# Optimization experiments

Measured on AMD Instinct MI355X. Metric: run time of the kernel, lower is better.

The kernel has to match this reference:

```python
import math
import jax, jax.numpy as jnp
import numpy as np

B, L, DIM, H = 2, 2048, 1024, 16
D = DIM // H  # head_dim = 64
EPS = 1e-6


def setup_inputs() -> dict:
    key = jax.random.key(0)
    ks = jax.random.split(key, 5)
    s = 0.02
    return {
        "x": jax.random.normal(ks[0], (B, L, DIM), jnp.float32),
        "pe": jax.random.normal(ks[1], (B, 1, L, D // 2, 2, 2), jnp.float32),
        "w_qkv": jax.random.normal(ks[2], (DIM, 3 * DIM), jnp.float32) * s,
        "q_scale": jnp.ones((D,), jnp.float32),
        "k_scale": jnp.ones((D,), jnp.float32),
        "w_proj": jax.random.normal(ks[3], (DIM, DIM), jnp.float32) * s,
        "b_proj": jnp.zeros((DIM,), jnp.float32),
    }


def _rmsnorm(t, scale):
    # flax nnx.RMSNorm: x * rsqrt(mean(x^2) + eps) * scale, over last dim
    var = jnp.mean(jnp.square(t), axis=-1, keepdims=True)
    return t * jax.lax.rsqrt(var + EPS) * scale


def _apply_rope(t, pe):
    # t: [B,H,L,D]; pe: [B,1,L,D/2,2,2]
    t2 = t.reshape(*t.shape[:-1], D // 2, 1, 2)
    out = pe[..., 0] * t2[..., 0] + pe[..., 1] * t2[..., 1]  # [B,H,L,D/2,2]
    return out.reshape(t.shape)


def reference(x, pe, w_qkv, q_scale, k_scale, w_proj, b_proj):
    # fused QKV projection
    qkv = jnp.einsum('bld,de->ble', x, w_qkv)  # [B,L,3*DIM]
    qkv = qkv.reshape(B, L, 3, H, D).transpose(2, 0, 3, 1, 4)  # [3,B,H,L,D]
    q, k, v = qkv[0], qkv[1], qkv[2]
    # QK RMSNorm
    q = _rmsnorm(q, q_scale)
    k = _rmsnorm(k, k_scale)
    # RoPE via pe
    q = _apply_rope(q, pe)
    k = _apply_rope(k, pe)
    # scaled dot product attention
    scores = jnp.einsum('bhqd,bhkd->bhqk', q, k) / math.sqrt(D)
    attn = jax.nn.softmax(scores, axis=-1)
    o = jnp.einsum('bhqk,bhkd->bhqd', attn, v)  # [B,H,L,D]
    o = o.transpose(0, 2, 1, 3).reshape(B, L, DIM)  # B H L D -> B L (H D)
    # output projection
    return jnp.einsum('bld,de->ble', o, w_proj) + b_proj
```

## Files before the change

kernel.cpp:

```cpp
#include <hip/hip_runtime.h>
#include <math.h>

#define BB 2
#define LL 2048
#define DIMM 1024
#define HH 16
#define DD 64
#define QKV_N 3072

typedef unsigned short u16;
typedef unsigned int u32;
typedef __attribute__((ext_vector_type(8))) short short8;
typedef __attribute__((ext_vector_type(4))) float f32x4;

__device__ __forceinline__ float bf2f(u16 h) {
    unsigned u = ((unsigned)h) << 16;
    return __uint_as_float(u);
}
__device__ __forceinline__ u16 f2bf(float f) {
    unsigned u = __float_as_uint(f);
    u += 0x7fffu + ((u >> 16) & 1u);
    return (u16)(u >> 16);
}
__device__ __forceinline__ u32 pack_bf2(float lo, float hi) {
    u32 a = __float_as_uint(hi) + 0x8000u;
    u32 b = __float_as_uint(lo) + 0x8000u;
    return __builtin_amdgcn_perm(a, b, 0x07060302u);
}
__device__ __forceinline__ void gload16(const u16* g, u16* l) {
    __builtin_amdgcn_global_load_lds(
        (const __attribute__((address_space(1))) void*)g,
        (__attribute__((address_space(3))) void*)l, 16, 0, 0);
}

__global__ __launch_bounds__(256) void convx(
    const float* __restrict__ X, u16* __restrict__ Af)
{
    const int g = blockIdx.x * 256 + threadIdx.x;
    const int lane = g & 63;
    const int frag = g >> 6;
    const int rt = frag >> 5;
    const int kts = (frag >> 1) & 15;
    const int ks2 = frag & 1;
    const int R = rt * 16 + (lane & 15);
    const int k = kts * 64 + ks2 * 32 + ((lane >> 4) & 3) * 8;
    float4 a = *(const float4*)&X[(size_t)R * DIMM + k];
    float4 b = *(const float4*)&X[(size_t)R * DIMM + k + 4];
    u16 t[8] = {f2bf(a.x), f2bf(a.y), f2bf(a.z), f2bf(a.w),
                f2bf(b.x), f2bf(b.y), f2bf(b.z), f2bf(b.w)};
    *(uint4*)&Af[(size_t)frag * 512 + lane * 8] = *(uint4*)t;
}

__global__ __launch_bounds__(256) void convt(
    const float* __restrict__ W, u16* __restrict__ Wt, int K, int N, int fragmode)
{
    __shared__ u16 s[64][72];
    const int tid = threadIdx.x;
    const int k0 = blockIdx.x * 64, n0 = blockIdx.y * 64;
#pragma unroll
    for (int t = 0; t < 16; ++t) {
        int flat = t * 256 + tid;
        int kk = flat >> 6, nn = flat & 63;
        s[nn][kk] = f2bf(W[(size_t)(k0 + kk) * N + n0 + nn]);
    }
    __syncthreads();
    if (fragmode) {
        const int kts = k0 >> 6;
        const int kdiv = K >> 6;
#pragma unroll
        for (int t2 = 0; t2 < 2; ++t2) {
            int idx = t2 * 256 + tid;
            int fpart = idx >> 6, lane_s = idx & 63;
            int ct = (n0 >> 4) + (fpart >> 1);
            int ks2 = fpart & 1;
            int nn = (fpart >> 1) * 16 + (lane_s & 15);
            int kk = ks2 * 32 + ((lane_s >> 4) & 3) * 8;
            *(uint4*)&Wt[((size_t)(ct * kdiv + kts) * 2 + ks2) * 512 + lane_s * 8]
                = *(const uint4*)&s[nn][kk];
        }
    } else {
#pragma unroll
        for (int t2 = 0; t2 < 2; ++t2) {
            int chunk = t2 * 256 + tid;
            int nn = chunk >> 3, kc = chunk & 7;
            *(uint4*)&Wt[(size_t)(n0 + nn) * K + k0 + kc * 8] = *(uint4*)&s[nn][kc * 8];
        }
    }
}

__global__ __launch_bounds__(256) void gemm_qkv(
    const u16* __restrict__ Af, const u16* __restrict__ Bf,
    u16* __restrict__ C, u16* __restrict__ kp, u16* __restrict__ vp,
    const float* __restrict__ pe,
    const float* __restrict__ qs, const float* __restrict__ ks)
{
    __shared__ u16 smem[16384];

    const int tid = threadIdx.x;
    const int wave = tid >> 6, lane = tid & 63;
    const int mIdx = lane & 15, quad = lane >> 4;
    const int wr = wave >> 1, wc = wave & 1;
    const int xcd = blockIdx.x & 7, lid = blockIdx.x >> 3;
    const int m0 = ((xcd & 3) * 8 + (lid & 7)) * 128;
    const int n0 = ((xcd >> 2) * 12 + (lid >> 3)) * 128;
    const int N = QKV_N;

    const u16* abase = Af + ((size_t)((m0 >> 4) + 4 * wr)) * 16384 + lane * 8;
    const u16* bbase = Bf + ((size_t)((n0 >> 4) + 4 * wc)) * 16384 + lane * 8;

    f32x4 acc[4][4];
#pragma unroll
    for (int a = 0; a < 4; ++a)
#pragma unroll
        for (int b = 0; b < 4; ++b) acc[a][b] = (f32x4){0.f, 0.f, 0.f, 0.f};

    short8 aA[4], bA[4], aB[4], bB[4];
#pragma unroll
    for (int i = 0; i < 4; ++i) {
        aA[i] = *(const short8*)&abase[(size_t)i * 16384];
        bA[i] = *(const short8*)&bbase[(size_t)i * 16384];
    }

    for (int t = 0; t < 16; ++t) {
        const size_t o1 = (size_t)t * 1024 + 512;
#pragma unroll
        for (int i = 0; i < 4; ++i) {
            aB[i] = *(const short8*)&abase[(size_t)i * 16384 + o1];
            bB[i] = *(const short8*)&bbase[(size_t)i * 16384 + o1];
        }
        __builtin_amdgcn_sched_barrier(0);
#pragma unroll
        for (int mt = 0; mt < 4; ++mt)
#pragma unroll
            for (int nt = 0; nt < 4; ++nt)
                acc[mt][nt] = __builtin_amdgcn_mfma_f32_16x16x32_bf16(
                    aA[mt], bA[nt], acc[mt][nt], 0, 0, 0);
        __builtin_amdgcn_sched_barrier(0);
        if (t + 1 < 16) {
            const size_t o0 = (size_t)(t + 1) * 1024;
#pragma unroll
            for (int i = 0; i < 4; ++i) {
                aA[i] = *(const short8*)&abase[(size_t)i * 16384 + o0];
                bA[i] = *(const short8*)&bbase[(size_t)i * 16384 + o0];
            }
        }
        __builtin_amdgcn_sched_barrier(0);
#pragma unroll
        for (int mt = 0; mt < 4; ++mt)
#pragma unroll
            for (int nt = 0; nt < 4; ++nt)
                acc[mt][nt] = __builtin_amdgcn_mfma_f32_16x16x32_bf16(
                    aB[mt], bB[nt], acc[mt][nt], 0, 0, 0);
        __builtin_amdgcn_sched_barrier(0);
    }

    if (n0 >= 2048) {
#pragma unroll
        for (int mt = 0; mt < 4; ++mt) {
            const int tl0 = 64 * wr + 16 * mt + 4 * quad;
#pragma unroll
            for (int nt = 0; nt < 4; ++nt) {
                const int d = 16 * nt + mIdx;
                const int lblk = ((wc * 2 + (tl0 >> 6)) * 4 + (d >> 4)) * 2
                                 + ((tl0 >> 5) & 1);
                const int ln = (d & 15) + 16 * ((tl0 >> 3) & 3);
                uint2 pr;
                pr.x = pack_bf2(acc[mt][nt][0], acc[mt][nt][1]);
                pr.y = pack_bf2(acc[mt][nt][2], acc[mt][nt][3]);
                *(uint2*)&smem[lblk * 512 + ln * 8 + (tl0 & 7)] = pr;
            }
        }
        __syncthreads();
        {
            const int b = m0 >> 11;
            const int h0 = (n0 - 2048) >> 6;
            const int ktb = (m0 & 2047) >> 6;
#pragma unroll
            for (int g2 = 0; g2 < 4; ++g2) {
                const int bh = b * 16 + h0 + (g2 >> 1);
                const int kt = ktb + (g2 & 1);
                u16* dst = vp + ((size_t)(bh * 32 + kt) * 8) * 512;
                const u16* src = &smem[g2 * 8 * 512];
#pragma unroll
                for (int ps = 0; ps < 2; ++ps) {
                    const int off = (ps * 256 + tid) * 8;
                    *(uint4*)&dst[off] = *(const uint4*)&src[off];
                }
            }
        }
    } else {
        const bool isq = (n0 < 1024);
        const float* scv = isq ? qs : ks;
        const float pre = isq ? 0.18033688011112042f : 1.0f;
        float scl[4];
#pragma unroll
        for (int nt = 0; nt < 4; ++nt) scl[nt] = scv[16 * nt + mIdx];

#pragma unroll
        for (int mt = 0; mt < 4; ++mt) {
#pragma unroll
            for (int r = 0; r < 4; ++r) {
                float s = 0.f;
#pragma unroll
                for (int nt = 0; nt < 4; ++nt) {
                    float a = acc[mt][nt][r];
                    s += a * a;
                }
                s += __shfl_xor(s, 1);
                s += __shfl_xor(s, 2);
                s += __shfl_xor(s, 4);
                s += __shfl_xor(s, 8);
                float rn = rsqrtf(s * (1.f / 64.f) + 1e-6f);
                const int tl = 64 * wr + 16 * mt + 4 * quad + r;
                const int R = m0 + tl;
                size_t peo = (size_t)R * 128;
#pragma unroll
                for (int nt = 0; nt < 4; ++nt) {
                    float v = acc[mt][nt][r] * rn * scl[nt];
                    float pp = __shfl_xor(v, 1);
                    float2 pw = *(const float2*)&pe[peo + 2 * (16 * nt + mIdx)];
                    float e  = (mIdx & 1) ? pp : v;
                    float od = (mIdx & 1) ? v : pp;
                    u16 val = f2bf((pw.x * e + pw.y * od) * pre);
                    if (isq) {
                        C[(size_t)R * N + n0 + 64 * wc + 16 * nt + mIdx] = val;
                    } else {
                        const int d = 16 * nt + mIdx;
                        const int lblk = ((wc * 2 + (tl >> 6)) * 4 + ((tl >> 4) & 3)) * 2
                                         + (d >> 5);
                        smem[lblk * 512 + ((tl & 15) + 16 * ((d >> 3) & 3)) * 8
                             + (d & 7)] = val;
                    }
                }
            }
        }
        if (!isq) {
            __syncthreads();
            const int b = m0 >> 11;
            const int h0 = (n0 - 1024) >> 6;
            const int ktb = (m0 & 2047) >> 6;
#pragma unroll
            for (int g2 = 0; g2 < 4; ++g2) {
                const int bh = b * 16 + h0 + (g2 >> 1);
                const int kt = ktb + (g2 & 1);
                u16* dst = kp + ((size_t)(bh * 32 + kt) * 8) * 512;
                const u16* src = &smem[g2 * 8 * 512];
#pragma unroll
                for (int ps = 0; ps < 2; ++ps) {
                    const int off = (ps * 256 + tid) * 8;
                    *(uint4*)&dst[off] = *(const uint4*)&src[off];
                }
            }
        }
    }
}

__global__ __launch_bounds__(256) void gemm_proj(
    const u16* __restrict__ A, const u16* __restrict__ Bt,
    const float* __restrict__ bias, float* __restrict__ C)
{
    __shared__ u16 smem[2 * 12288];

    const int tid = threadIdx.x;
    const int wave = tid >> 6, lane = tid & 63;
    const int mIdx = lane & 15, quad = lane >> 4;
    const int wr = wave >> 1, wc = wave & 1;
    const int xcd = blockIdx.x & 7, lid = blockIdx.x >> 3;
    const int m0 = (xcd * 8 + (lid >> 3)) * 64;
    const int n0 = (lid & 7) * 128;
    const int N = DIMM, K = DIMM;
    const int lr = lane >> 3, lc = lane & 7;

    f32x4 acc[2][4];
#pragma unroll
    for (int a = 0; a < 2; ++a)
#pragma unroll
        for (int b = 0; b < 4; ++b) acc[a][b] = (f32x4){0.f, 0.f, 0.f, 0.f};

    auto stage = [&](int buf, int k0) {
        u16* sA = smem + buf * 12288;
        u16* sB = sA + 4096;
#pragma unroll
        for (int j = 0; j < 2; ++j) {
            int r0 = 16 * wave + 8 * j + lr;
            gload16(&A[(size_t)(m0 + r0) * K + k0 + 8 * (lc ^ lr)],
                    &sA[(16 * wave + 8 * j) * 64]);
        }
#pragma unroll
        for (int j = 0; j < 4; ++j) {
            int r0 = 32 * wave + 8 * j + lr;
            gload16(&Bt[(size_t)(n0 + r0) * K + k0 + 8 * (lc ^ lr)],
                    &sB[(32 * wave + 8 * j) * 64]);
        }
    };

    stage(0, 0);
    __syncthreads();
    int cur = 0;
    for (int t = 0; t < 16; ++t) {
        if (t + 1 < 16) stage(cur ^ 1, (t + 1) * 64);
        const u16* sA = smem + cur * 12288;
        const u16* sB = sA + 4096;
#pragma unroll
        for (int ks2 = 0; ks2 < 2; ++ks2) {
            short8 af[2], bfr[4];
#pragma unroll
            for (int mt = 0; mt < 2; ++mt) {
                int Ra = 32 * wr + 16 * mt + mIdx;
                af[mt] = *(const short8*)&sA[Ra * 64 + 8 * ((ks2 * 4 + quad) ^ (Ra & 7))];
            }
#pragma unroll
            for (int nt = 0; nt < 4; ++nt) {
                int Rb = 64 * wc + 16 * nt + mIdx;
                bfr[nt] = *(const short8*)&sB[Rb * 64 + 8 * ((ks2 * 4 + quad) ^ (Rb & 7))];
            }
#pragma unroll
            for (int mt = 0; mt < 2; ++mt)
#pragma unroll
                for (int nt = 0; nt < 4; ++nt)
                    acc[mt][nt] = __builtin_amdgcn_mfma_f32_16x16x32_bf16(
                        af[mt], bfr[nt], acc[mt][nt], 0, 0, 0);
        }
        __syncthreads();
        cur ^= 1;
    }

#pragma unroll
    for (int mt = 0; mt < 2; ++mt)
#pragma unroll
        for (int r = 0; r < 4; ++r) {
            int row = m0 + 32 * wr + 16 * mt + quad * 4 + r;
#pragma unroll
            for (int nt = 0; nt < 4; ++nt) {
                int col = n0 + 64 * wc + 16 * nt + mIdx;
                C[(size_t)row * N + col] = acc[mt][nt][r] + bias[col];
            }
        }
}

__global__ __launch_bounds__(256, 2) void attn_mfma(
    const u16* __restrict__ qkv, const u16* __restrict__ kp,
    const u16* __restrict__ vp, u16* __restrict__ o)
{
    __shared__ u16 sP[128 * 64];

    const int tid = threadIdx.x;
    const int wave = tid >> 6;
    const int lane = tid & 63;
    const int mIdx = lane & 15;
    const int quad = lane >> 4;
    const int m7 = mIdx & 7;

    const int bid = ((blockIdx.x & 7) << 6) | (blockIdx.x >> 3);
    const int bh = bid >> 4;
    const int qt = bid & 15;
    const int b = bh >> 4, h = bh & 15;
    const int q0 = qt * 128;

    const u16* kbase = kp + (size_t)bh * 32 * 4096 + lane * 8;
    const u16* vbase = vp + (size_t)bh * 32 * 4096 + lane * 8;

    short8 aq[2][2];
#pragma unroll
    for (int g = 0; g < 2; ++g) {
        const u16* qrow = qkv + (size_t)b * LL * QKV_N + h * 64
                          + (size_t)(q0 + 32 * wave + 16 * g + mIdx) * QKV_N;
        aq[g][0] = *(const short8*)&qrow[quad * 8];
        aq[g][1] = *(const short8*)&qrow[32 + quad * 8];
    }

    const short8 bones = {(short)0x3F80, (short)0x3F80, (short)0x3F80, (short)0x3F80,
                          (short)0x3F80, (short)0x3F80, (short)0x3F80, (short)0x3F80};

    f32x4 Oacc[2][4];
    f32x4 lac[2];
#pragma unroll
    for (int g = 0; g < 2; ++g) {
        lac[g] = (f32x4){0.f, 0.f, 0.f, 0.f};
#pragma unroll
        for (int nb = 0; nb < 4; ++nb) Oacc[g][nb] = (f32x4){0.f, 0.f, 0.f, 0.f};
    }

    const int o0 = 8 * (quad ^ m7);
    const int o1 = 8 * ((quad + 4) ^ m7);
    u16* sPr0 = &sP[(32 * wave + mIdx) * 64];
    u16* sPr1 = &sP[(32 * wave + 16 + mIdx) * 64];

    short8 kfA[8], kfB[8], vf[8];

#pragma unroll
    for (int f = 0; f < 8; ++f) kfA[f] = *(const short8*)&kbase[f * 512];

    auto body = [&](short8* KC, short8* KN, int kt) {
        const size_t tb = (size_t)kt * 4096;
#pragma unroll
        for (int f = 0; f < 8; ++f) vf[f] = *(const short8*)&vbase[tb + f * 512];
        if (kt < 31) {
#pragma unroll
            for (int f = 0; f < 8; ++f) KN[f] = *(const short8*)&kbase[tb + 4096 + f * 512];
        }
        __builtin_amdgcn_sched_barrier(0);

#pragma unroll
        for (int nb = 0; nb < 4; ++nb) {
            const int pofs = (16 * nb + 4 * quad) ^ (8 * m7);
#pragma unroll
            for (int g = 0; g < 2; ++g) {
                f32x4 st = (f32x4){0.f, 0.f, 0.f, 0.f};
                st = __builtin_amdgcn_mfma_f32_16x16x32_bf16(KC[nb * 2 + 0], aq[g][0], st, 0, 0, 0);
                st = __builtin_amdgcn_mfma_f32_16x16x32_bf16(KC[nb * 2 + 1], aq[g][1], st, 0, 0, 0);
                float p0 = exp2f(st[0]), p1 = exp2f(st[1]);
                float p2 = exp2f(st[2]), p3 = exp2f(st[3]);
                uint2 wp;
                wp.x = pack_bf2(p0, p1);
                wp.y = pack_bf2(p2, p3);
                *(uint2*)&((g == 0 ? sPr0 : sPr1)[pofs]) = wp;
            }
        }
        short8 pa00 = *(const short8*)&sPr0[o0];
        short8 pa01 = *(const short8*)&sPr0[o1];
        short8 pa10 = *(const short8*)&sPr1[o0];
        short8 pa11 = *(const short8*)&sPr1[o1];

        lac[0] = __builtin_amdgcn_mfma_f32_16x16x32_bf16(pa00, bones, lac[0], 0, 0, 0);
        lac[0] = __builtin_amdgcn_mfma_f32_16x16x32_bf16(pa01, bones, lac[0], 0, 0, 0);
        lac[1] = __builtin_amdgcn_mfma_f32_16x16x32_bf16(pa10, bones, lac[1], 0, 0, 0);
        lac[1] = __builtin_amdgcn_mfma_f32_16x16x32_bf16(pa11, bones, lac[1], 0, 0, 0);

        __builtin_amdgcn_s_setprio(1);
#pragma unroll
        for (int nb = 0; nb < 4; ++nb) {
            Oacc[0][nb] = __builtin_amdgcn_mfma_f32_16x16x32_bf16(pa00, vf[nb * 2 + 0], Oacc[0][nb], 0, 0, 0);
            Oacc[0][nb] = __builtin_amdgcn_mfma_f32_16x16x32_bf16(pa01, vf[nb * 2 + 1], Oacc[0][nb], 0, 0, 0);
            Oacc[1][nb] = __builtin_amdgcn_mfma_f32_16x16x32_bf16(pa10, vf[nb * 2 + 0], Oacc[1][nb], 0, 0, 0);
            Oacc[1][nb] = __builtin_amdgcn_mfma_f32_16x16x32_bf16(pa11, vf[nb * 2 + 1], Oacc[1][nb], 0, 0, 0);
        }
        __builtin_amdgcn_s_setprio(0);
    };

    for (int kt2 = 0; kt2 < 16; ++kt2) {
        body(kfA, kfB, 2 * kt2);
        body(kfB, kfA, 2 * kt2 + 1);
    }

#pragma unroll
    for (int g = 0; g < 2; ++g)
#pragma unroll
        for (int r = 0; r < 4; ++r) {
            float linv = 1.f / lac[g][r];
            const int rowg = b * LL + q0 + 32 * wave + 16 * g + quad * 4 + r;
#pragma unroll
            for (int nb = 0; nb < 4; ++nb) {
                o[(size_t)rowg * DIMM + h * 64 + 16 * nb + mIdx] =
                    f2bf(Oacc[g][nb][r] * linv);
            }
        }
}

extern "C" void kernel_launch(void* const* d_in, const int* in_sizes, int n_in,
                              void* d_out, int out_size, void* d_ws, size_t ws_size,
                              hipStream_t stream) {
    const float* x       = (const float*)d_in[0];
    const float* pe      = (const float*)d_in[1];
    const float* w_qkv   = (const float*)d_in[2];
    const float* q_scale = (const float*)d_in[3];
    const float* k_scale = (const float*)d_in[4];
    const float* w_proj  = (const float*)d_in[5];
    const float* b_proj  = (const float*)d_in[6];
    float* out = (float*)d_out;

    char* ws = (char*)d_ws;
    u16* qkv    = (u16*)ws;  ws += (size_t)4096 * 3072 * 2;
    u16* o      = (u16*)ws;  ws += (size_t)4096 * 1024 * 2;
    u16* xb     = (u16*)ws;  ws += (size_t)4096 * 1024 * 2;
    u16* wqkvt  = (u16*)ws;  ws += (size_t)3072 * 1024 * 2;
    u16* wprojt = (u16*)ws;  ws += (size_t)1024 * 1024 * 2;
    u16* kpack  = (u16*)ws;  ws += (size_t)32 * 32 * 4096 * 2;
    u16* vpack  = (u16*)ws;  ws += (size_t)32 * 32 * 4096 * 2;

    convx<<<(4096 * 1024) / (256 * 8), 256, 0, stream>>>(x, xb);
    convt<<<dim3(1024 / 64, QKV_N / 64), 256, 0, stream>>>(w_qkv, wqkvt, DIMM, QKV_N, 1);
    convt<<<dim3(1024 / 64, 1024 / 64), 256, 0, stream>>>(w_proj, wprojt, DIMM, DIMM, 0);

    gemm_qkv<<<768, 256, 0, stream>>>(
        xb, wqkvt, qkv, kpack, vpack, pe, q_scale, k_scale);

    attn_mfma<<<BB * HH * (LL / 128), 256, 0, stream>>>(qkv, kpack, vpack, o);

    gemm_proj<<<512, 256, 0, stream>>>(o, wprojt, b_proj, out);
}
```

Baseline: 221.4 us.

## Split QKV GEMM into per-region templated launches and stage Q stores via LDS

Replaces the single QKV GEMM launch with three template-specialized launches, one each for the Q, K and V column regions, so region branches resolve at compile time. The block-to-tile mapping changes so that each XCD covers a contiguous M range across all 8 N blocks of a region. Q output is now staged through padded shared memory and written as coalesced 16-byte row stores instead of scattered 2-byte stores. The cost is two extra kernel launches and 256-block grids that may underfill the GPU and serialize the three regions.

Result: faster. 209.5 us (-5.4%).

```diff
diff --git a/kernel.cpp b/kernel.cpp
--- a/kernel.cpp
+++ b/kernel.cpp
@@ -88,21 +88,23 @@
     }
 }
 
-__global__ __launch_bounds__(256) void gemm_qkv(
+template<int REGION>
+__global__ __launch_bounds__(256) void gemm_qkv_r(
     const u16* __restrict__ Af, const u16* __restrict__ Bf,
     u16* __restrict__ C, u16* __restrict__ kp, u16* __restrict__ vp,
     const float* __restrict__ pe,
     const float* __restrict__ qs, const float* __restrict__ ks)
 {
-    __shared__ u16 smem[16384];
+    __shared__ u16 smem[REGION == 0 ? 128 * 136 : 16384];
 
     const int tid = threadIdx.x;
     const int wave = tid >> 6, lane = tid & 63;
     const int mIdx = lane & 15, quad = lane >> 4;
     const int wr = wave >> 1, wc = wave & 1;
     const int xcd = blockIdx.x & 7, lid = blockIdx.x >> 3;
-    const int m0 = ((xcd & 3) * 8 + (lid & 7)) * 128;
-    const int n0 = ((xcd >> 2) * 12 + (lid >> 3)) * 128;
+    const int m0 = (xcd * 4 + (lid >> 3)) * 128;
+    const int nblk = lid & 7;
+    const int n0 = REGION * 1024 + nblk * 128;
     const int N = QKV_N;
 
     const u16* abase = Af + ((size_t)((m0 >> 4) + 4 * wr)) * 16384 + lane * 8;
@@ -154,7 +156,7 @@
         __builtin_amdgcn_sched_barrier(0);
     }
 
-    if (n0 >= 2048) {
+    if constexpr (REGION == 2) {
 #pragma unroll
         for (int mt = 0; mt < 4; ++mt) {
             const int tl0 = 64 * wr + 16 * mt + 4 * quad;
@@ -173,7 +175,7 @@
         __syncthreads();
         {
             const int b = m0 >> 11;
-            const int h0 = (n0 - 2048) >> 6;
+            const int h0 = nblk * 2;
             const int ktb = (m0 & 2047) >> 6;
 #pragma unroll
             for (int g2 = 0; g2 < 4; ++g2) {
@@ -189,9 +191,8 @@
             }
         }
     } else {
-        const bool isq = (n0 < 1024);
-        const float* scv = isq ? qs : ks;
-        const float pre = isq ? 0.18033688011112042f : 1.0f;
+        const float* scv = (REGION == 0) ? qs : ks;
+        const float pre = (REGION == 0) ? 0.18033688011112042f : 1.0f;
         float scl[4];
 #pragma unroll
         for (int nt = 0; nt < 4; ++nt) scl[nt] = scv[16 * nt + mIdx];
@@ -222,8 +223,8 @@
                     float e  = (mIdx & 1) ? pp : v;
                     float od = (mIdx & 1) ? v : pp;
                     u16 val = f2bf((pw.x * e + pw.y * od) * pre);
-                    if (isq) {
-                        C[(size_t)R * N + n0 + 64 * wc + 16 * nt + mIdx] = val;
+                    if constexpr (REGION == 0) {
+                        smem[tl * 136 + 64 * wc + 16 * nt + mIdx] = val;
                     } else {
                         const int d = 16 * nt + mIdx;
                         const int lblk = ((wc * 2 + (tl >> 6)) * 4 + ((tl >> 4) & 3)) * 2
@@ -234,10 +235,17 @@
                 }
             }
         }
-        if (!isq) {
-            __syncthreads();
+        __syncthreads();
+        if constexpr (REGION == 0) {
+            const int row = tid >> 1, half = tid & 1;
+            u16* dst = C + (size_t)(m0 + row) * QKV_N + n0 + half * 64;
+            const u16* src = &smem[row * 136 + half * 64];
+#pragma unroll
+            for (int c = 0; c < 8; ++c)
+                *(uint4*)&dst[c * 8] = *(const uint4*)&src[c * 8];
+        } else {
             const int b = m0 >> 11;
-            const int h0 = (n0 - 1024) >> 6;
+            const int h0 = nblk * 2;
             const int ktb = (m0 & 2047) >> 6;
 #pragma unroll
             for (int g2 = 0; g2 < 4; ++g2) {
@@ -482,8 +490,9 @@
     convt<<<dim3(1024 / 64, QKV_N / 64), 256, 0, stream>>>(w_qkv, wqkvt, DIMM, QKV_N, 1);
     convt<<<dim3(1024 / 64, 1024 / 64), 256, 0, stream>>>(w_proj, wprojt, DIMM, DIMM, 0);
 
-    gemm_qkv<<<768, 256, 0, stream>>>(
-        xb, wqkvt, qkv, kpack, vpack, pe, q_scale, k_scale);
+    gemm_qkv_r<0><<<256, 256, 0, stream>>>(xb, wqkvt, qkv, kpack, vpack, pe, q_scale, k_scale);
+    gemm_qkv_r<1><<<256, 256, 0, stream>>>(xb, wqkvt, qkv, kpack, vpack, pe, q_scale, k_scale);
+    gemm_qkv_r<2><<<256, 256, 0, stream>>>(xb, wqkvt, qkv, kpack, vpack, pe, q_scale, k_scale);
 
     attn_mfma<<<BB * HH * (LL / 128), 256, 0, stream>>>(qkv, kpack, vpack, o);
 
```
